# Kernel tuning notes

Measured on AMD Instinct MI355X. Metric: run time of the kernel, lower is better.

The kernel has to match this reference:

```python
import jax, jax.numpy as jnp
import numpy as np

V = 32000   # vocab
D = 512     # embed dim
H = 512     # hidden dim
K = 5       # beam size
SOS, EOS, PAD = 0, 1, 2
NEG = -1e30  # acts as -inf but keeps grads NaN-free


def gru_cell(x, h, Wih, Whh, bih, bhh):
    # torch nn.GRU cell convention: gates ordered (r, z, n)
    gi = x @ Wih.T + bih
    gh = h @ Whh.T + bhh
    i_r, i_z, i_n = jnp.split(gi, 3, axis=-1)
    h_r, h_z, h_n = jnp.split(gh, 3, axis=-1)
    r = jax.nn.sigmoid(i_r + h_r)
    z = jax.nn.sigmoid(i_z + h_z)
    n = jnp.tanh(i_n + r * h_n)
    return (1.0 - z) * n + z * h


def setup_inputs() -> dict:
    key = jax.random.key(0)
    ks = jax.random.split(key, 14)
    s = 0.02
    f = jnp.float32
    return {
        "source": jax.random.randint(ks[0], (32, 32), 0, V, dtype=jnp.int32),
        "emb_src": jax.random.normal(ks[1], (V, D), f) * s,
        "emb_tgt": jax.random.normal(ks[2], (V, D), f) * s,
        "enc_Wih": jax.random.normal(ks[3], (3 * H, D), f) * s,
        "enc_Whh": jax.random.normal(ks[4], (3 * H, H), f) * s,
        "enc_bih": jnp.zeros((3 * H,), f),
        "enc_bhh": jnp.zeros((3 * H,), f),
        "dec_Wih": jax.random.normal(ks[5], (3 * H, D), f) * s,
        "dec_Whh": jax.random.normal(ks[6], (3 * H, H), f) * s,
        "dec_bih": jnp.zeros((3 * H,), f),
        "dec_bhh": jnp.zeros((3 * H,), f),
        "W_out": jax.random.normal(ks[7], (H, V), f) * s,
        "b_out": jnp.zeros((V,), f),
    }


def beam_search(source, emb_src, emb_tgt, enc_Wih, enc_Whh, enc_bih, enc_bhh,
                dec_Wih, dec_Whh, dec_bih, dec_bhh, W_out, b_out):
    B, S = source.shape
    T = S + 1  # max decode steps (while counter < source.shape[1] + 1)

    # ---- encoder: 1-layer GRU over source tokens ----
    xs = jnp.swapaxes(emb_src[source], 0, 1)  # [S, B, D]
    def enc_step(h, x):
        return gru_cell(x, h, enc_Wih, enc_Whh, enc_bih, enc_bhh), None
    h_enc, _ = jax.lax.scan(enc_step, jnp.zeros((B, H), xs.dtype), xs)
    # initialize_h: repeat each sentence's hidden state beam_size times
    hidden = jnp.broadcast_to(h_enc[:, None, :], (B, K, H))  # [B, K, H]

    def dec_logprobs(tok, hid):
        x = emb_tgt[tok]  # [B, K, D]
        h1 = gru_cell(x, hid, dec_Wih, dec_Whh, dec_bih, dec_bhh)
        lp = jax.nn.log_softmax(h1 @ W_out + b_out, axis=-1)  # [B, K, V]
        return lp, h1

    # ---- step 0: initial_advance (top-K words from one SOS row) ----
    lp, h1 = dec_logprobs(jnp.zeros((B, K), jnp.int32), hidden)
    vals, words = jax.lax.top_k(lp[:, 0, :], K)  # [B, K]
    seqs = jnp.full((B, K, T + 1), PAD, jnp.int32)
    seqs = seqs.at[:, :, 0].set(SOS).at[:, :, 1].set(words)
    act_ll = vals
    hidden = h1  # all beams identical at step 0
    best_ll = jnp.full((B,), NEG, vals.dtype)
    best_seq = jnp.full((B, T + 1), PAD, jnp.int32)
    pos = jnp.arange(T + 1)
    bidx = jnp.arange(B)

    # ---- steps 1..T-1: advance. Dead beam slots carry NEG likelihood,
    # which reproduces the shrinking-active-set math of the original. ----
    def step(carry, t):
        seqs, act_ll, hidden, last_tok, best_ll, best_seq = carry
        lp, h1 = dec_logprobs(last_tok, hidden)
        L = (act_ll[:, :, None] + lp).reshape(B, K * V)
        vals, idx = jax.lax.top_k(L, K)
        parent = idx // V           # seq_ind
        word = idx % V              # word_ind
        gathered = jnp.take_along_axis(seqs, parent[:, :, None], axis=1)
        new_seqs = jnp.where(pos[None, None, :] == t + 1, word[:, :, None], gathered)
        finite = vals > NEG * 0.5
        is_eos = (word == EOS) & finite
        # completed likelihood normalized by candidate length (t+2 tokens)
        comp_ll = jnp.where(is_eos, vals / (t.astype(vals.dtype) + 2.0), NEG)
        cbest = comp_ll.max(axis=1)
        cseq = new_seqs[bidx, comp_ll.argmax(axis=1)]  # [B, T+1], PAD-padded
        improve = cbest > best_ll
        best_ll = jnp.where(improve, cbest, best_ll)
        best_seq = jnp.where(improve[:, None], cseq, best_seq)
        act_ll = jnp.where(finite & ~is_eos, vals, NEG)
        hidden = jnp.take_along_axis(h1, parent[:, :, None], axis=1)  # arrange_h gather
        return (new_seqs, act_ll, hidden, word, best_ll, best_seq), None

    carry = (seqs, act_ll, hidden, words, best_ll, best_seq)
    carry, _ = jax.lax.scan(step, carry, jnp.arange(1, T))
    seqs, act_ll, hidden, last_tok, best_ll, best_seq = carry

    # return_winner: best completed if any, else best active
    have = best_ll > NEG * 0.5
    act_best = act_ll.argmax(axis=1)
    act_seq = seqs[bidx, act_best]
    winner = jnp.where(have[:, None], best_seq, act_seq)  # [B, T+1]
    winner_ll = jnp.where(have, best_ll, act_ll.max(axis=1))
    return winner, winner_ll


def reference(source, emb_src, emb_tgt, enc_Wih, enc_Whh, enc_bih, enc_bhh,
              dec_Wih, dec_Whh, dec_bih, dec_bhh, W_out, b_out):
    winner, _ = beam_search(source, emb_src, emb_tgt, enc_Wih, enc_Whh, enc_bih,
                            enc_bhh, dec_Wih, dec_Whh, dec_bih, dec_bhh, W_out, b_out)
    return winner
```

## Files before the change

### kernel.cpp

```cpp
#include <hip/hip_runtime.h>
#include <math.h>

#define NEGF   (-1e30f)
#define FINTH  (-5e29f)
#define VSZ    32000
#define KBM    5
#define SEQL   34
#define NVBLK  1000

__device__ __forceinline__ bool cand_gt(float av, int ai, float bv, int bi) {
  return (av > bv) || (av == bv && ai < bi);
}

#define INS5(xx, ii)                                                           \
  if (cand_gt(xx, ii, tv4, ti4)) {                                             \
    tv4 = xx; ti4 = ii;                                                        \
    if (cand_gt(tv4, ti4, tv3, ti3)) { float tf = tv3; int tj = ti3; tv3 = tv4; ti3 = ti4; tv4 = tf; ti4 = tj; \
      if (cand_gt(tv3, ti3, tv2, ti2)) { tf = tv2; tj = ti2; tv2 = tv3; ti2 = ti3; tv3 = tf; ti3 = tj; \
        if (cand_gt(tv2, ti2, tv1, ti1)) { tf = tv1; tj = ti1; tv1 = tv2; ti1 = ti2; tv2 = tf; ti2 = tj; \
          if (cand_gt(tv1, ti1, tv0, ti0)) { tf = tv0; tj = ti0; tv0 = tv1; ti0 = ti1; tv1 = tf; ti1 = tj; } } } } }

__global__ void init_kernel(float* hb0, int* word_buf, int* hsrc) {
  int i = blockIdx.x * 256 + threadIdx.x;
  if (i < 32 * 512) hb0[i] = 0.f;
  if (i < 160) { word_buf[i] = 0; hsrc[i] = i / KBM; }
}

__global__ __launch_bounds__(256, 4) void genc_kernel(
    const float* __restrict__ emb, const int* __restrict__ source,
    const float* __restrict__ Wih, float* __restrict__ gi_enc)
{
  const int tid = threadIdx.x;
  const int ng = tid & 7;
  const int mg = tid >> 3;
  const int j0 = blockIdx.x * 16 + ng * 2;
  const int r0 = blockIdx.y * 128 + mg * 4;

  const float* arow[4];
  #pragma unroll
  for (int i = 0; i < 4; i++) {
    int r = r0 + i;
    int tok = source[(r & 31) * 32 + (r >> 5)];
    arow[i] = emb + (long)tok * 512;
  }
  const float* w0p = Wih + (long)j0 * 512;
  const float* w1p = w0p + 512;

  float acc0[4], acc1[4];
  #pragma unroll
  for (int i = 0; i < 4; i++) { acc0[i] = 0.f; acc1[i] = 0.f; }

  float4 wc0 = *(const float4*)w0p;
  float4 wc1 = *(const float4*)w1p;
  float4 ac[4];
  #pragma unroll
  for (int i = 0; i < 4; i++) ac[i] = *(const float4*)arow[i];

  for (int k = 0; k < 508; k += 4) {
    float4 wn0 = *(const float4*)(w0p + k + 4);
    float4 wn1 = *(const float4*)(w1p + k + 4);
    float4 an[4];
    #pragma unroll
    for (int i = 0; i < 4; i++) an[i] = *(const float4*)(arow[i] + k + 4);
    #pragma unroll
    for (int i = 0; i < 4; i++) {
      acc0[i] += ac[i].x * wc0.x + ac[i].y * wc0.y + ac[i].z * wc0.z + ac[i].w * wc0.w;
      acc1[i] += ac[i].x * wc1.x + ac[i].y * wc1.y + ac[i].z * wc1.z + ac[i].w * wc1.w;
    }
    wc0 = wn0; wc1 = wn1;
    #pragma unroll
    for (int i = 0; i < 4; i++) ac[i] = an[i];
  }
  #pragma unroll
  for (int i = 0; i < 4; i++) {
    acc0[i] += ac[i].x * wc0.x + ac[i].y * wc0.y + ac[i].z * wc0.z + ac[i].w * wc0.w;
    acc1[i] += ac[i].x * wc1.x + ac[i].y * wc1.y + ac[i].z * wc1.z + ac[i].w * wc1.w;
  }
  #pragma unroll
  for (int i = 0; i < 4; i++) {
    float2 r; r.x = acc0[i]; r.y = acc1[i];
    *(float2*)(gi_enc + (long)(r0 + i) * 1536 + j0) = r;
  }
}

template<int P, int HONLY>
__global__ __launch_bounds__(256, 4) void gates_kernel(
    const float* __restrict__ emb, const int* __restrict__ tok_ptr, int tok_stride,
    const float* __restrict__ hbuf, const int* __restrict__ hsrc,
    const float* __restrict__ Wih, const float* __restrict__ Whh,
    float* __restrict__ gip, float* __restrict__ ghp)
{
  const bool is_h = HONLY ? true : (blockIdx.y != 0);
  const float* W = is_h ? Whh : Wih;
  const int M = 32 * P;
  float* out = (is_h ? ghp : gip) + (long)blockIdx.z * M * 1536;

  const int tid = threadIdx.x;
  const int ng = tid & 7;
  const int mg = tid >> 3;
  const int j0 = blockIdx.x * 16 + ng * 2;
  const int k0 = blockIdx.z * 128;

  const float* arow[P];
  #pragma unroll
  for (int i = 0; i < P; i++) {
    int m = mg * P + i;
    if (is_h) { int r = hsrc ? hsrc[m] : m; arow[i] = hbuf + (long)r * 512 + k0; }
    else      { int tk = tok_ptr[m * tok_stride]; arow[i] = emb + (long)tk * 512 + k0; }
  }
  const float* w0p = W + (long)j0 * 512 + k0;
  const float* w1p = w0p + 512;

  float acc0[P], acc1[P];
  #pragma unroll
  for (int i = 0; i < P; i++) { acc0[i] = 0.f; acc1[i] = 0.f; }

  float4 wc0 = *(const float4*)w0p;
  float4 wc1 = *(const float4*)w1p;
  float4 ac[P];
  #pragma unroll
  for (int i = 0; i < P; i++) ac[i] = *(const float4*)arow[i];

  for (int k = 0; k < 124; k += 4) {
    float4 wn0 = *(const float4*)(w0p + k + 4);
    float4 wn1 = *(const float4*)(w1p + k + 4);
    float4 an[P];
    #pragma unroll
    for (int i = 0; i < P; i++) an[i] = *(const float4*)(arow[i] + k + 4);
    #pragma unroll
    for (int i = 0; i < P; i++) {
      acc0[i] += ac[i].x * wc0.x + ac[i].y * wc0.y + ac[i].z * wc0.z + ac[i].w * wc0.w;
      acc1[i] += ac[i].x * wc1.x + ac[i].y * wc1.y + ac[i].z * wc1.z + ac[i].w * wc1.w;
    }
    wc0 = wn0; wc1 = wn1;
    #pragma unroll
    for (int i = 0; i < P; i++) ac[i] = an[i];
  }
  #pragma unroll
  for (int i = 0; i < P; i++) {
    acc0[i] += ac[i].x * wc0.x + ac[i].y * wc0.y + ac[i].z * wc0.z + ac[i].w * wc0.w;
    acc1[i] += ac[i].x * wc1.x + ac[i].y * wc1.y + ac[i].z * wc1.z + ac[i].w * wc1.w;
  }
  #pragma unroll
  for (int i = 0; i < P; i++) {
    int m = mg * P + i;
    float2 r; r.x = acc0[i]; r.y = acc1[i];
    *(float2*)(out + (long)m * 1536 + j0) = r;
  }
}

template<int NPI, int NPH, int M>
__global__ __launch_bounds__(256) void hupd_kernel(
    const float* __restrict__ gip, const float* __restrict__ ghp,
    const float* __restrict__ bih, const float* __restrict__ bhh,
    const float* __restrict__ hin, const int* __restrict__ hsrc,
    float* __restrict__ hout)
{
  int idx = blockIdx.x * 256 + threadIdx.x;
  if (idx >= M * 512) return;
  int m = idx >> 9, i = idx & 511;
  float ir = 0.f, iz = 0.f, inn = 0.f, hr = 0.f, hz = 0.f, hn = 0.f;
  #pragma unroll
  for (int p = 0; p < NPI; p++) {
    const float* g = gip + (long)p * M * 1536 + (long)m * 1536;
    ir += g[i]; iz += g[512 + i]; inn += g[1024 + i];
  }
  #pragma unroll
  for (int p = 0; p < NPH; p++) {
    const float* g = ghp + (long)p * M * 1536 + (long)m * 1536;
    hr += g[i]; hz += g[512 + i]; hn += g[1024 + i];
  }
  ir += bih[i]; iz += bih[512 + i]; inn += bih[1024 + i];
  hr += bhh[i]; hz += bhh[512 + i]; hn += bhh[1024 + i];
  float r = 1.f / (1.f + expf(-(ir + hr)));
  float z = 1.f / (1.f + expf(-(iz + hz)));
  float n = tanhf(inn + r * hn);
  int src = hsrc ? hsrc[m] : m;
  float h = hin[(long)src * 512 + i];
  hout[(long)m * 512 + i] = (1.f - z) * n + z * h;
}

__global__ __launch_bounds__(256, 4) void logtop_kernel(
    const float* __restrict__ h1, const float* __restrict__ Wout,
    const float* __restrict__ bout,
    float* __restrict__ pms, float* __restrict__ pv, int* __restrict__ pi)
{
  const int tid = threadIdx.x;
  const int ng = tid & 7;
  const int mg = tid >> 3;
  const int blk = blockIdx.x;
  const int v0 = blk * 32;
  const int v = v0 + ng * 4;
  const int m0 = mg * 5;

  __shared__ float Wlds[2][2048];
  __shared__ float L[160][33];

  const float* a0 = h1 + (long)m0 * 512;

  const int skk = tid >> 3;
  const int sv4 = tid & 7;
  const float* sg0 = Wout + (size_t)skk * VSZ + v0 + sv4 * 4;
  const float* sg1 = Wout + (size_t)(32 + skk) * VSZ + v0 + sv4 * 4;
  const int lwave = (tid >> 6) * 256;

  auto stage = [&](int tt, int bb) {
    const float* g0 = sg0 + (size_t)tt * 64 * VSZ;
    const float* g1 = sg1 + (size_t)tt * 64 * VSZ;
    __builtin_amdgcn_global_load_lds(
        (const __attribute__((address_space(1))) void*)g0,
        (__attribute__((address_space(3))) void*)&Wlds[bb][lwave], 16, 0, 0);
    __builtin_amdgcn_global_load_lds(
        (const __attribute__((address_space(1))) void*)g1,
        (__attribute__((address_space(3))) void*)&Wlds[bb][1024 + lwave], 16, 0, 0);
  };

  float4 acc[5];
  #pragma unroll
  for (int i = 0; i < 5; i++) acc[i] = make_float4(0.f, 0.f, 0.f, 0.f);

  stage(0, 0);
  __syncthreads();

  float4 aA[5], aB[5];
  #pragma unroll
  for (int i = 0; i < 5; i++) aA[i] = *(const float4*)(a0 + i * 512);

  for (int t8 = 0; t8 < 8; t8++) {
    const float* lb = &Wlds[t8 & 1][0];
    if (t8 < 7) stage(t8 + 1, (t8 + 1) & 1);
    const int kt = t8 * 64;
    #pragma unroll 1
    for (int c = 0; c < 16; c += 2) {
      const int k = kt + c * 4;
      float4 w0[4], w1[4];
      #pragma unroll
      for (int j = 0; j < 4; j++) w0[j] = *(const float4*)&lb[(c * 4 + j) * 32 + ng * 4];
      #pragma unroll
      for (int j = 0; j < 4; j++) w1[j] = *(const float4*)&lb[(c * 4 + 4 + j) * 32 + ng * 4];
      #pragma unroll
      for (int i = 0; i < 5; i++) aB[i] = *(const float4*)(a0 + i * 512 + k + 4);
      #pragma unroll
      for (int i = 0; i < 5; i++) {
        acc[i].x += aA[i].x * w0[0].x + aA[i].y * w0[1].x + aA[i].z * w0[2].x + aA[i].w * w0[3].x;
        acc[i].y += aA[i].x * w0[0].y + aA[i].y * w0[1].y + aA[i].z * w0[2].y + aA[i].w * w0[3].y;
        acc[i].z += aA[i].x * w0[0].z + aA[i].y * w0[1].z + aA[i].z * w0[2].z + aA[i].w * w0[3].z;
        acc[i].w += aA[i].x * w0[0].w + aA[i].y * w0[1].w + aA[i].z * w0[2].w + aA[i].w * w0[3].w;
      }
      int kn = k + 8; if (kn >= 512) kn = 0;
      #pragma unroll
      for (int i = 0; i < 5; i++) aA[i] = *(const float4*)(a0 + i * 512 + kn);
      #pragma unroll
      for (int i = 0; i < 5; i++) {
        acc[i].x += aB[i].x * w1[0].x + aB[i].y * w1[1].x + aB[i].z * w1[2].x + aB[i].w * w1[3].x;
        acc[i].y += aB[i].x * w1[0].y + aB[i].y * w1[1].y + aB[i].z * w1[2].y + aB[i].w * w1[3].y;
        acc[i].z += aB[i].x * w1[0].z + aB[i].y * w1[1].z + aB[i].z * w1[2].z + aB[i].w * w1[3].z;
        acc[i].w += aB[i].x * w1[0].w + aB[i].y * w1[1].w + aB[i].z * w1[2].w + aB[i].w * w1[3].w;
      }
    }
    __syncthreads();
  }

  float4 bb4 = *(const float4*)(bout + v);
  #pragma unroll
  for (int i = 0; i < 5; i++) {
    L[m0 + i][ng * 4 + 0] = acc[i].x + bb4.x;
    L[m0 + i][ng * 4 + 1] = acc[i].y + bb4.y;
    L[m0 + i][ng * 4 + 2] = acc[i].z + bb4.z;
    L[m0 + i][ng * 4 + 3] = acc[i].w + bb4.w;
  }
  __syncthreads();

  if (tid < 160) {
    float m = -3.4e38f, s = 0.f;
    float tv0 = -3.4e38f, tv1 = -3.4e38f, tv2 = -3.4e38f, tv3 = -3.4e38f, tv4 = -3.4e38f;
    int ti0 = 0x7fffffff, ti1 = 0x7fffffff, ti2 = 0x7fffffff, ti3 = 0x7fffffff, ti4 = 0x7fffffff;
    int base = blk * 32;
    for (int c = 0; c < 32; c++) {
      float x = L[tid][c];
      if (x > m) { s *= expf(m - x); m = x; }
      s += expf(x - m);
      INS5(x, base + c);
    }
    long o = (long)blk * 160 + tid;
    pms[o * 2 + 0] = m; pms[o * 2 + 1] = s;
    pv[o * 5 + 0] = tv0; pi[o * 5 + 0] = ti0;
    pv[o * 5 + 1] = tv1; pi[o * 5 + 1] = ti1;
    pv[o * 5 + 2] = tv2; pi[o * 5 + 2] = ti2;
    pv[o * 5 + 3] = tv3; pi[o * 5 + 3] = ti3;
    pv[o * 5 + 4] = tv4; pi[o * 5 + 4] = ti4;
  }
}

__global__ __launch_bounds__(256) void merge_kernel(
    const float* __restrict__ pms, const float* __restrict__ pv,
    const int* __restrict__ pi, float* __restrict__ lse,
    float* __restrict__ rv5, int* __restrict__ ri5)
{
  int row = blockIdx.x, tid = threadIdx.x;
  float m = -3.4e38f, s = 0.f;
  float tv0 = -3.4e38f, tv1 = -3.4e38f, tv2 = -3.4e38f, tv3 = -3.4e38f, tv4 = -3.4e38f;
  int ti0 = 0x7fffffff, ti1 = 0x7fffffff, ti2 = 0x7fffffff, ti3 = 0x7fffffff, ti4 = 0x7fffffff;

  for (int blk = tid; blk < NVBLK; blk += 256) {
    long o = (long)blk * 160 + row;
    float bm = pms[o * 2 + 0], bs = pms[o * 2 + 1];
    float nm = fmaxf(m, bm);
    s = s * expf(m - nm) + bs * expf(bm - nm);
    m = nm;
    float xv; int xi;
    xv = pv[o * 5 + 0]; xi = pi[o * 5 + 0]; INS5(xv, xi);
    xv = pv[o * 5 + 1]; xi = pi[o * 5 + 1]; INS5(xv, xi);
    xv = pv[o * 5 + 2]; xi = pi[o * 5 + 2]; INS5(xv, xi);
    xv = pv[o * 5 + 3]; xi = pi[o * 5 + 3]; INS5(xv, xi);
    xv = pv[o * 5 + 4]; xi = pi[o * 5 + 4]; INS5(xv, xi);
  }
  for (int mask = 1; mask < 64; mask <<= 1) {
    float om = __shfl_xor(m, mask, 64);
    float os = __shfl_xor(s, mask, 64);
    float nm = fmaxf(m, om);
    s = s * expf(m - nm) + os * expf(om - nm);
    m = nm;
  }
  __shared__ float sm[4], ss[4];
  __shared__ float sv[256 * 5];
  __shared__ int   si[256 * 5];
  if ((tid & 63) == 0) { sm[tid >> 6] = m; ss[tid >> 6] = s; }
  sv[tid * 5 + 0] = tv0; si[tid * 5 + 0] = ti0;
  sv[tid * 5 + 1] = tv1; si[tid * 5 + 1] = ti1;
  sv[tid * 5 + 2] = tv2; si[tid * 5 + 2] = ti2;
  sv[tid * 5 + 3] = tv3; si[tid * 5 + 3] = ti3;
  sv[tid * 5 + 4] = tv4; si[tid * 5 + 4] = ti4;
  __syncthreads();
  if (tid == 0) {
    float M2 = sm[0], S2 = ss[0];
    for (int w = 1; w < 4; w++) {
      float nm = fmaxf(M2, sm[w]);
      S2 = S2 * expf(M2 - nm) + ss[w] * expf(sm[w] - nm);
      M2 = nm;
    }
    lse[row] = M2 + logf(S2);
  }
  for (int str = 128; str >= 1; str >>= 1) {
    if (tid < str) {
      float* av = &sv[tid * 5];         int* ai = &si[tid * 5];
      float* bv = &sv[(tid + str) * 5]; int* bi = &si[(tid + str) * 5];
      float o0[5]; int o1[5];
      int i = 0, j = 0;
      #pragma unroll
      for (int o = 0; o < 5; o++) {
        float avv = av[i]; int aii = ai[i];
        float bvv = bv[j]; int bii = bi[j];
        bool ta = cand_gt(avv, aii, bvv, bii);
        o0[o] = ta ? avv : bvv; o1[o] = ta ? aii : bii;
        i += ta ? 1 : 0; j += ta ? 0 : 1;
      }
      #pragma unroll
      for (int o = 0; o < 5; o++) { av[o] = o0[o]; ai[o] = o1[o]; }
    }
    __syncthreads();
  }
  if (tid == 0) {
    #pragma unroll
    for (int o = 0; o < 5; o++) { rv5[row * 5 + o] = sv[o]; ri5[row * 5 + o] = si[o]; }
  }
}

__global__ void book0_kernel(const float* __restrict__ rv5, const int* __restrict__ ri5,
                             const float* __restrict__ lse,
                             int* __restrict__ seqs, float* __restrict__ act_ll,
                             int* __restrict__ word_buf, int* __restrict__ hsrc,
                             float* __restrict__ best_ll, int* __restrict__ best_seq)
{
  int b = blockIdx.x, tid = threadIdx.x;
  int row = b * KBM;
  float l = lse[row];
  if (tid < SEQL) {
    for (int j = 0; j < KBM; j++) {
      int w = ri5[row * 5 + j];
      seqs[(b * KBM + j) * SEQL + tid] = (tid == 0) ? 0 : (tid == 1 ? w : 2);
    }
    best_seq[b * SEQL + tid] = 2;
  }
  if (tid < KBM) {
    act_ll[b * KBM + tid] = rv5[row * 5 + tid] - l;
    word_buf[b * KBM + tid] = ri5[row * 5 + tid];
    hsrc[b * KBM + tid] = b * KBM + tid;
  }
  if (tid == 0) best_ll[b] = NEGF;
}

__global__ void book_kernel(const float* __restrict__ rv5, const int* __restrict__ ri5,
                            const float* __restrict__ lse,
                            const int* __restrict__ seqs_old, int* __restrict__ seqs_new,
                            float* __restrict__ act_ll, int* __restrict__ word_buf,
                            int* __restrict__ hsrc, float* __restrict__ best_ll,
                            int* __restrict__ best_seq, int t)
{
  int b = blockIdx.x, tid = threadIdx.x;
  __shared__ float sv5[5];
  __shared__ int   si5[5];
  if (tid == 0) {
    float tv0 = -3.4e38f, tv1 = -3.4e38f, tv2 = -3.4e38f, tv3 = -3.4e38f, tv4 = -3.4e38f;
    int ti0 = 0x7fffffff, ti1 = 0x7fffffff, ti2 = 0x7fffffff, ti3 = 0x7fffffff, ti4 = 0x7fffffff;
    for (int k = 0; k < KBM; k++) {
      int row = b * KBM + k;
      float a = act_ll[row], l = lse[row];
      #pragma unroll
      for (int j = 0; j < 5; j++) {
        float x = a + (rv5[row * 5 + j] - l);
        int id = k * VSZ + ri5[row * 5 + j];
        INS5(x, id);
      }
    }
    sv5[0] = tv0; si5[0] = ti0; sv5[1] = tv1; si5[1] = ti1;
    sv5[2] = tv2; si5[2] = ti2; sv5[3] = tv3; si5[3] = ti3;
    sv5[4] = tv4; si5[4] = ti4;
  }
  __syncthreads();

  __shared__ int ls[KBM][SEQL];
  float v[KBM]; int pr[KBM], wd[KBM];
  #pragma unroll
  for (int j = 0; j < KBM; j++) {
    v[j] = sv5[j];
    int id = si5[j];
    pr[j] = id / VSZ; wd[j] = id % VSZ;
  }
  #pragma unroll
  for (int j = 0; j < KBM; j++) {
    if (tid < SEQL) {
      int x = (tid == t + 1) ? wd[j] : seqs_old[(b * KBM + pr[j]) * SEQL + tid];
      ls[j][tid] = x;
      seqs_new[(b * KBM + j) * SEQL + tid] = x;
    }
  }
  __syncthreads();
  float cll[KBM];
  #pragma unroll
  for (int j = 0; j < KBM; j++) {
    bool fin = v[j] > FINTH;
    bool eos = (wd[j] == 1) && fin;
    cll[j] = eos ? v[j] / (float)(t + 2) : NEGF;
  }
  int jb = 0; float cb = cll[0];
  #pragma unroll
  for (int j = 1; j < KBM; j++) if (cll[j] > cb) { cb = cll[j]; jb = j; }
  bool improve = cb > best_ll[b];
  if (improve) {
    if (tid == 0) best_ll[b] = cb;
    if (tid < SEQL) best_seq[b * SEQL + tid] = ls[jb][tid];
  }
  if (tid < KBM) {
    int j = tid;
    bool fin = v[j] > FINTH;
    bool eos = (wd[j] == 1) && fin;
    act_ll[b * KBM + j] = (fin && !eos) ? v[j] : NEGF;
    word_buf[b * KBM + j] = wd[j];
    hsrc[b * KBM + j] = b * KBM + pr[j];
  }
}

__global__ void final_kernel(const float* __restrict__ best_ll, const int* __restrict__ best_seq,
                             const float* __restrict__ act_ll, const int* __restrict__ seqs,
                             int* __restrict__ out)
{
  int b = blockIdx.x, tid = threadIdx.x;
  bool have = best_ll[b] > FINTH;
  int jb = 0; float ab = act_ll[b * KBM];
  for (int j = 1; j < KBM; j++)
    if (act_ll[b * KBM + j] > ab) { ab = act_ll[b * KBM + j]; jb = j; }
  if (tid < SEQL)
    out[b * SEQL + tid] = have ? best_seq[b * SEQL + tid]
                               : seqs[(b * KBM + jb) * SEQL + tid];
}

extern "C" void kernel_launch(void* const* d_in, const int* in_sizes, int n_in,
                              void* d_out, int out_size, void* d_ws, size_t ws_size,
                              hipStream_t stream)
{
  const int*   source  = (const int*)d_in[0];
  const float* emb_src = (const float*)d_in[1];
  const float* emb_tgt = (const float*)d_in[2];
  const float* eWih = (const float*)d_in[3];
  const float* eWhh = (const float*)d_in[4];
  const float* ebih = (const float*)d_in[5];
  const float* ebhh = (const float*)d_in[6];
  const float* dWih = (const float*)d_in[7];
  const float* dWhh = (const float*)d_in[8];
  const float* dbih = (const float*)d_in[9];
  const float* dbhh = (const float*)d_in[10];
  const float* Wout = (const float*)d_in[11];
  const float* bout = (const float*)d_in[12];
  int* out = (int*)d_out;

  char* ws = (char*)d_ws;
  size_t off = 0;
  auto alloc = [&](size_t bytes) {
    void* p = ws + off;
    off = (off + bytes + 255) & ~(size_t)255;
    return p;
  };
  float* hb0     = (float*)alloc(160 * 512 * 4);
  float* hb1     = (float*)alloc(160 * 512 * 4);
  float* gip     = (float*)alloc((size_t)4 * 160 * 1536 * 4);
  float* ghp     = (float*)alloc((size_t)4 * 160 * 1536 * 4);
  char*  uni     = (char*) alloc((size_t)8 * 1024 * 1024);
  float* gi_enc  = (float*)uni;
  float* pms     = (float*)uni;
  float* pv      = (float*)(uni + 1536 * 1024);
  int*   pi      = (int*)  (uni + 1536 * 1024 + 3328 * 1024);
  float* lse     = (float*)alloc(160 * 4);
  float* act_ll  = (float*)alloc(160 * 4);
  float* rv5     = (float*)alloc(160 * 5 * 4);
  float* best_ll = (float*)alloc(32 * 4);
  int*   ri5     = (int*)alloc(160 * 5 * 4);
  int*   seqs0   = (int*)alloc(160 * SEQL * 4);
  int*   seqs1   = (int*)alloc(160 * SEQL * 4);
  int*   wordb   = (int*)alloc(160 * 4);
  int*   hsrc    = (int*)alloc(160 * 4);
  int*   bseq    = (int*)alloc(32 * SEQL * 4);

  init_kernel<<<64, 256, 0, stream>>>(hb0, wordb, hsrc);

  genc_kernel<<<dim3(96, 8), 256, 0, stream>>>(emb_src, source, eWih, gi_enc);
  for (int s = 0; s < 32; s++) {
    gates_kernel<1, 1><<<dim3(96, 1, 4), 256, 0, stream>>>(
        nullptr, nullptr, 0, hb0, nullptr, nullptr, eWhh, nullptr, ghp);
    hupd_kernel<1, 4, 32><<<64, 256, 0, stream>>>(
        gi_enc + (size_t)s * 32 * 1536, ghp, ebih, ebhh, hb0, nullptr, hb0);
  }

  gates_kernel<5, 0><<<dim3(96, 2, 4), 256, 0, stream>>>(
      emb_tgt, wordb, 1, hb0, hsrc, dWih, dWhh, gip, ghp);
  hupd_kernel<4, 4, 160><<<320, 256, 0, stream>>>(
      gip, ghp, dbih, dbhh, hb0, hsrc, hb1);
  logtop_kernel<<<NVBLK, 256, 0, stream>>>(hb1, Wout, bout, pms, pv, pi);
  merge_kernel<<<160, 256, 0, stream>>>(pms, pv, pi, lse, rv5, ri5);
  book0_kernel<<<32, 64, 0, stream>>>(rv5, ri5, lse, seqs0, act_ll, wordb, hsrc,
                                      best_ll, bseq);

  float* hcur = hb1; float* hoth = hb0;
  int* scur = seqs0; int* soth = seqs1;
  for (int t = 1; t <= 32; t++) {
    gates_kernel<5, 0><<<dim3(96, 2, 4), 256, 0, stream>>>(
        emb_tgt, wordb, 1, hcur, hsrc, dWih, dWhh, gip, ghp);
    hupd_kernel<4, 4, 160><<<320, 256, 0, stream>>>(
        gip, ghp, dbih, dbhh, hcur, hsrc, hoth);
    logtop_kernel<<<NVBLK, 256, 0, stream>>>(hoth, Wout, bout, pms, pv, pi);
    merge_kernel<<<160, 256, 0, stream>>>(pms, pv, pi, lse, rv5, ri5);
    book_kernel<<<32, 64, 0, stream>>>(rv5, ri5, lse, scur, soth, act_ll, wordb,
                                       hsrc, best_ll, bseq, t);
    { float* tmp = hcur; hcur = hoth; hoth = tmp; }
    { int* tmp = scur; scur = soth; soth = tmp; }
  }

  final_kernel<<<32, 64, 0, stream>>>(best_ll, bseq, act_ll, scur, out);
}
```

Measured before the change: 6.886 ms.

## Fuse merge and beam bookkeeping into one kernel with packed partials

Merges the per-row top-5/logsumexp reduction kernel and the beam bookkeeping kernel into a single per-sentence kernel, using wave shuffles for the reduction instead of a shared-memory tree. The logits kernel now writes its partials as a packed 16-float record per row, read back with float4 loads. This removes one launch per decode step and the intermediate lse/top-5 buffers. The trade-off is only 32 blocks doing the merge work, each handling 5 rows per thread. The encoder input-projection kernel also gets half the rows per thread and twice the grid.

New measurement: 10.30 ms. 49.5% more time.

```diff
diff --git a/kernel.cpp b/kernel.cpp
--- a/kernel.cpp
+++ b/kernel.cpp
@@ -20,6 +20,41 @@
         if (cand_gt(tv2, ti2, tv1, ti1)) { tf = tv1; tj = ti1; tv1 = tv2; ti1 = ti2; tv2 = tf; ti2 = tj; \
           if (cand_gt(tv1, ti1, tv0, ti0)) { tf = tv0; tj = ti0; tv0 = tv1; ti0 = ti1; tv1 = tf; ti1 = tj; } } } } }
 
+struct T5 { float v[5]; int i[5]; };
+
+__device__ __forceinline__ void t5_init(T5& t) {
+  #pragma unroll
+  for (int j = 0; j < 5; j++) { t.v[j] = -3.4e38f; t.i[j] = 0x7fffffff; }
+}
+
+__device__ __forceinline__ void t5_ins(T5& t, float x, int id) {
+  if (cand_gt(x, id, t.v[4], t.i[4])) {
+    t.v[4] = x; t.i[4] = id;
+    #pragma unroll
+    for (int j = 4; j > 0; j--) {
+      if (cand_gt(t.v[j], t.i[j], t.v[j-1], t.i[j-1])) {
+        float tf = t.v[j-1]; int tj = t.i[j-1];
+        t.v[j-1] = t.v[j]; t.i[j-1] = t.i[j];
+        t.v[j] = tf; t.i[j] = tj;
+      }
+    }
+  }
+}
+
+__device__ __forceinline__ T5 t5_merge(const T5& a, const T5& b) {
+  T5 r;
+  int i = 0, j = 0;
+  #pragma unroll
+  for (int o = 0; o < 5; o++) {
+    float avv = a.v[i]; int aii = a.i[i];
+    float bvv = b.v[j]; int bii = b.i[j];
+    bool ta = cand_gt(avv, aii, bvv, bii);
+    r.v[o] = ta ? avv : bvv; r.i[o] = ta ? aii : bii;
+    i += ta ? 1 : 0; j += ta ? 0 : 1;
+  }
+  return r;
+}
+
 __global__ void init_kernel(float* hb0, int* word_buf, int* hsrc) {
   int i = blockIdx.x * 256 + threadIdx.x;
   if (i < 32 * 512) hb0[i] = 0.f;
@@ -34,11 +69,11 @@
   const int ng = tid & 7;
   const int mg = tid >> 3;
   const int j0 = blockIdx.x * 16 + ng * 2;
-  const int r0 = blockIdx.y * 128 + mg * 4;
-
-  const float* arow[4];
-  #pragma unroll
-  for (int i = 0; i < 4; i++) {
+  const int r0 = blockIdx.y * 64 + mg * 2;
+
+  const float* arow[2];
+  #pragma unroll
+  for (int i = 0; i < 2; i++) {
     int r = r0 + i;
     int tok = source[(r & 31) * 32 + (r >> 5)];
     arow[i] = emb + (long)tok * 512;
@@ -46,38 +81,38 @@
   const float* w0p = Wih + (long)j0 * 512;
   const float* w1p = w0p + 512;
 
-  float acc0[4], acc1[4];
-  #pragma unroll
-  for (int i = 0; i < 4; i++) { acc0[i] = 0.f; acc1[i] = 0.f; }
+  float acc0[2], acc1[2];
+  #pragma unroll
+  for (int i = 0; i < 2; i++) { acc0[i] = 0.f; acc1[i] = 0.f; }
 
   float4 wc0 = *(const float4*)w0p;
   float4 wc1 = *(const float4*)w1p;
-  float4 ac[4];
-  #pragma unroll
-  for (int i = 0; i < 4; i++) ac[i] = *(const float4*)arow[i];
+  float4 ac[2];
+  #pragma unroll
+  for (int i = 0; i < 2; i++) ac[i] = *(const float4*)arow[i];
 
   for (int k = 0; k < 508; k += 4) {
     float4 wn0 = *(const float4*)(w0p + k + 4);
     float4 wn1 = *(const float4*)(w1p + k + 4);
-    float4 an[4];
-    #pragma unroll
-    for (int i = 0; i < 4; i++) an[i] = *(const float4*)(arow[i] + k + 4);
-    #pragma unroll
-    for (int i = 0; i < 4; i++) {
+    float4 an[2];
+    #pragma unroll
+    for (int i = 0; i < 2; i++) an[i] = *(const float4*)(arow[i] + k + 4);
+    #pragma unroll
+    for (int i = 0; i < 2; i++) {
       acc0[i] += ac[i].x * wc0.x + ac[i].y * wc0.y + ac[i].z * wc0.z + ac[i].w * wc0.w;
       acc1[i] += ac[i].x * wc1.x + ac[i].y * wc1.y + ac[i].z * wc1.z + ac[i].w * wc1.w;
     }
     wc0 = wn0; wc1 = wn1;
     #pragma unroll
-    for (int i = 0; i < 4; i++) ac[i] = an[i];
-  }
-  #pragma unroll
-  for (int i = 0; i < 4; i++) {
+    for (int i = 0; i < 2; i++) ac[i] = an[i];
+  }
+  #pragma unroll
+  for (int i = 0; i < 2; i++) {
     acc0[i] += ac[i].x * wc0.x + ac[i].y * wc0.y + ac[i].z * wc0.z + ac[i].w * wc0.w;
     acc1[i] += ac[i].x * wc1.x + ac[i].y * wc1.y + ac[i].z * wc1.z + ac[i].w * wc1.w;
   }
   #pragma unroll
-  for (int i = 0; i < 4; i++) {
+  for (int i = 0; i < 2; i++) {
     float2 r; r.x = acc0[i]; r.y = acc1[i];
     *(float2*)(gi_enc + (long)(r0 + i) * 1536 + j0) = r;
   }
@@ -182,8 +217,7 @@
 
 __global__ __launch_bounds__(256, 4) void logtop_kernel(
     const float* __restrict__ h1, const float* __restrict__ Wout,
-    const float* __restrict__ bout,
-    float* __restrict__ pms, float* __restrict__ pv, int* __restrict__ pi)
+    const float* __restrict__ bout, float* __restrict__ PK)
 {
   const int tid = threadIdx.x;
   const int ng = tid & 7;
@@ -282,182 +316,178 @@
       s += expf(x - m);
       INS5(x, base + c);
     }
-    long o = (long)blk * 160 + tid;
-    pms[o * 2 + 0] = m; pms[o * 2 + 1] = s;
-    pv[o * 5 + 0] = tv0; pi[o * 5 + 0] = ti0;
-    pv[o * 5 + 1] = tv1; pi[o * 5 + 1] = ti1;
-    pv[o * 5 + 2] = tv2; pi[o * 5 + 2] = ti2;
-    pv[o * 5 + 3] = tv3; pi[o * 5 + 3] = ti3;
-    pv[o * 5 + 4] = tv4; pi[o * 5 + 4] = ti4;
-  }
-}
-
-__global__ __launch_bounds__(256) void merge_kernel(
-    const float* __restrict__ pms, const float* __restrict__ pv,
-    const int* __restrict__ pi, float* __restrict__ lse,
-    float* __restrict__ rv5, int* __restrict__ ri5)
-{
-  int row = blockIdx.x, tid = threadIdx.x;
-  float m = -3.4e38f, s = 0.f;
-  float tv0 = -3.4e38f, tv1 = -3.4e38f, tv2 = -3.4e38f, tv3 = -3.4e38f, tv4 = -3.4e38f;
-  int ti0 = 0x7fffffff, ti1 = 0x7fffffff, ti2 = 0x7fffffff, ti3 = 0x7fffffff, ti4 = 0x7fffffff;
-
-  for (int blk = tid; blk < NVBLK; blk += 256) {
-    long o = (long)blk * 160 + row;
-    float bm = pms[o * 2 + 0], bs = pms[o * 2 + 1];
-    float nm = fmaxf(m, bm);
-    s = s * expf(m - nm) + bs * expf(bm - nm);
-    m = nm;
-    float xv; int xi;
-    xv = pv[o * 5 + 0]; xi = pi[o * 5 + 0]; INS5(xv, xi);
-    xv = pv[o * 5 + 1]; xi = pi[o * 5 + 1]; INS5(xv, xi);
-    xv = pv[o * 5 + 2]; xi = pi[o * 5 + 2]; INS5(xv, xi);
-    xv = pv[o * 5 + 3]; xi = pi[o * 5 + 3]; INS5(xv, xi);
-    xv = pv[o * 5 + 4]; xi = pi[o * 5 + 4]; INS5(xv, xi);
-  }
-  for (int mask = 1; mask < 64; mask <<= 1) {
-    float om = __shfl_xor(m, mask, 64);
-    float os = __shfl_xor(s, mask, 64);
-    float nm = fmaxf(m, om);
-    s = s * expf(m - nm) + os * expf(om - nm);
-    m = nm;
-  }
-  __shared__ float sm[4], ss[4];
-  __shared__ float sv[256 * 5];
-  __shared__ int   si[256 * 5];
-  if ((tid & 63) == 0) { sm[tid >> 6] = m; ss[tid >> 6] = s; }
-  sv[tid * 5 + 0] = tv0; si[tid * 5 + 0] = ti0;
-  sv[tid * 5 + 1] = tv1; si[tid * 5 + 1] = ti1;
-  sv[tid * 5 + 2] = tv2; si[tid * 5 + 2] = ti2;
-  sv[tid * 5 + 3] = tv3; si[tid * 5 + 3] = ti3;
-  sv[tid * 5 + 4] = tv4; si[tid * 5 + 4] = ti4;
-  __syncthreads();
-  if (tid == 0) {
-    float M2 = sm[0], S2 = ss[0];
-    for (int w = 1; w < 4; w++) {
-      float nm = fmaxf(M2, sm[w]);
-      S2 = S2 * expf(M2 - nm) + ss[w] * expf(sm[w] - nm);
-      M2 = nm;
-    }
-    lse[row] = M2 + logf(S2);
-  }
-  for (int str = 128; str >= 1; str >>= 1) {
-    if (tid < str) {
-      float* av = &sv[tid * 5];         int* ai = &si[tid * 5];
-      float* bv = &sv[(tid + str) * 5]; int* bi = &si[(tid + str) * 5];
-      float o0[5]; int o1[5];
-      int i = 0, j = 0;
-      #pragma unroll
-      for (int o = 0; o < 5; o++) {
-        float avv = av[i]; int aii = ai[i];
-        float bvv = bv[j]; int bii = bi[j];
-        bool ta = cand_gt(avv, aii, bvv, bii);
-        o0[o] = ta ? avv : bvv; o1[o] = ta ? aii : bii;
-        i += ta ? 1 : 0; j += ta ? 0 : 1;
-      }
-      #pragma unroll
-      for (int o = 0; o < 5; o++) { av[o] = o0[o]; ai[o] = o1[o]; }
-    }
-    __syncthreads();
-  }
-  if (tid == 0) {
-    #pragma unroll
-    for (int o = 0; o < 5; o++) { rv5[row * 5 + o] = sv[o]; ri5[row * 5 + o] = si[o]; }
-  }
-}
-
-__global__ void book0_kernel(const float* __restrict__ rv5, const int* __restrict__ ri5,
-                             const float* __restrict__ lse,
-                             int* __restrict__ seqs, float* __restrict__ act_ll,
-                             int* __restrict__ word_buf, int* __restrict__ hsrc,
-                             float* __restrict__ best_ll, int* __restrict__ best_seq)
-{
-  int b = blockIdx.x, tid = threadIdx.x;
-  int row = b * KBM;
-  float l = lse[row];
-  if (tid < SEQL) {
-    for (int j = 0; j < KBM; j++) {
-      int w = ri5[row * 5 + j];
-      seqs[(b * KBM + j) * SEQL + tid] = (tid == 0) ? 0 : (tid == 1 ? w : 2);
-    }
-    best_seq[b * SEQL + tid] = 2;
-  }
-  if (tid < KBM) {
-    act_ll[b * KBM + tid] = rv5[row * 5 + tid] - l;
-    word_buf[b * KBM + tid] = ri5[row * 5 + tid];
-    hsrc[b * KBM + tid] = b * KBM + tid;
-  }
-  if (tid == 0) best_ll[b] = NEGF;
-}
-
-__global__ void book_kernel(const float* __restrict__ rv5, const int* __restrict__ ri5,
-                            const float* __restrict__ lse,
-                            const int* __restrict__ seqs_old, int* __restrict__ seqs_new,
-                            float* __restrict__ act_ll, int* __restrict__ word_buf,
-                            int* __restrict__ hsrc, float* __restrict__ best_ll,
-                            int* __restrict__ best_seq, int t)
-{
-  int b = blockIdx.x, tid = threadIdx.x;
+    float* pk = PK + ((long)blk * 160 + tid) * 16;
+    float4 q0 = make_float4(m, s, tv0, tv1);
+    float4 q1 = make_float4(tv2, tv3, tv4, __int_as_float(ti0));
+    float4 q2 = make_float4(__int_as_float(ti1), __int_as_float(ti2),
+                            __int_as_float(ti3), __int_as_float(ti4));
+    *(float4*)(pk + 0) = q0;
+    *(float4*)(pk + 4) = q1;
+    *(float4*)(pk + 8) = q2;
+  }
+}
+
+template<int NR>
+__global__ __launch_bounds__(256) void mergebook_kernel(
+    const float* __restrict__ PK,
+    const int* __restrict__ seqs_old, int* __restrict__ seqs_new,
+    float* __restrict__ act_ll, int* __restrict__ word_buf,
+    int* __restrict__ hsrc, float* __restrict__ best_ll,
+    int* __restrict__ best_seq, int t)
+{
+  const int b = blockIdx.x, tid = threadIdx.x;
+
+  float m_[NR], s_[NR];
+  T5 t5[NR];
+  #pragma unroll
+  for (int k = 0; k < NR; k++) { m_[k] = -3.4e38f; s_[k] = 0.f; t5_init(t5[k]); }
+
+  for (int it = 0; it < 4; it++) {
+    int blk = tid + it * 256;
+    if (blk >= NVBLK) break;
+    #pragma unroll
+    for (int k = 0; k < NR; k++) {
+      const float* pk = PK + ((long)blk * 160 + b * KBM + k) * 16;
+      float4 q0 = *(const float4*)(pk + 0);
+      float4 q1 = *(const float4*)(pk + 4);
+      float4 q2 = *(const float4*)(pk + 8);
+      float nm = fmaxf(m_[k], q0.x);
+      s_[k] = s_[k] * expf(m_[k] - nm) + q0.y * expf(q0.x - nm);
+      m_[k] = nm;
+      t5_ins(t5[k], q0.z, __float_as_int(q1.w));
+      t5_ins(t5[k], q0.w, __float_as_int(q2.x));
+      t5_ins(t5[k], q1.x, __float_as_int(q2.y));
+      t5_ins(t5[k], q1.y, __float_as_int(q2.z));
+      t5_ins(t5[k], q1.z, __float_as_int(q2.w));
+    }
+  }
+
+  #pragma unroll
+  for (int k = 0; k < NR; k++) {
+    float m = m_[k], s = s_[k];
+    for (int mask = 1; mask < 64; mask <<= 1) {
+      float om = __shfl_xor(m, mask, 64);
+      float os = __shfl_xor(s, mask, 64);
+      float nm = fmaxf(m, om);
+      s = s * expf(m - nm) + os * expf(om - nm);
+      m = nm;
+    }
+    m_[k] = m; s_[k] = s;
+    for (int mask = 1; mask < 64; mask <<= 1) {
+      T5 o;
+      #pragma unroll
+      for (int j = 0; j < 5; j++) {
+        o.v[j] = __shfl_xor(t5[k].v[j], mask, 64);
+        o.i[j] = __shfl_xor(t5[k].i[j], mask, 64);
+      }
+      t5[k] = t5_merge(t5[k], o);
+    }
+  }
+
+  __shared__ float wm[KBM][4], wss[KBM][4], wv[KBM][4][5];
+  __shared__ int   wi[KBM][4][5];
   __shared__ float sv5[5];
   __shared__ int   si5[5];
+  const int wave = tid >> 6;
+  if ((tid & 63) == 0) {
+    #pragma unroll
+    for (int k = 0; k < NR; k++) {
+      wm[k][wave] = m_[k]; wss[k][wave] = s_[k];
+      #pragma unroll
+      for (int j = 0; j < 5; j++) { wv[k][wave][j] = t5[k].v[j]; wi[k][wave][j] = t5[k].i[j]; }
+    }
+  }
+  __syncthreads();
+
   if (tid == 0) {
-    float tv0 = -3.4e38f, tv1 = -3.4e38f, tv2 = -3.4e38f, tv3 = -3.4e38f, tv4 = -3.4e38f;
-    int ti0 = 0x7fffffff, ti1 = 0x7fffffff, ti2 = 0x7fffffff, ti3 = 0x7fffffff, ti4 = 0x7fffffff;
-    for (int k = 0; k < KBM; k++) {
-      int row = b * KBM + k;
-      float a = act_ll[row], l = lse[row];
+    T5 g; t5_init(g);
+    #pragma unroll
+    for (int k = 0; k < NR; k++) {
+      float M2 = wm[k][0], S2 = wss[k][0];
+      #pragma unroll
+      for (int w = 1; w < 4; w++) {
+        float nm = fmaxf(M2, wm[k][w]);
+        S2 = S2 * expf(M2 - nm) + wss[k][w] * expf(wm[k][w] - nm);
+        M2 = nm;
+      }
+      float l = M2 + logf(S2);
+      T5 rk;
+      #pragma unroll
+      for (int j = 0; j < 5; j++) { rk.v[j] = wv[k][0][j]; rk.i[j] = wi[k][0][j]; }
+      #pragma unroll
+      for (int w = 1; w < 4; w++) {
+        T5 o;
+        #pragma unroll
+        for (int j = 0; j < 5; j++) { o.v[j] = wv[k][w][j]; o.i[j] = wi[k][w][j]; }
+        rk = t5_merge(rk, o);
+      }
+      float a = (NR == 1) ? 0.f : act_ll[b * KBM + k];
       #pragma unroll
       for (int j = 0; j < 5; j++) {
-        float x = a + (rv5[row * 5 + j] - l);
-        int id = k * VSZ + ri5[row * 5 + j];
-        INS5(x, id);
-      }
-    }
-    sv5[0] = tv0; si5[0] = ti0; sv5[1] = tv1; si5[1] = ti1;
-    sv5[2] = tv2; si5[2] = ti2; sv5[3] = tv3; si5[3] = ti3;
-    sv5[4] = tv4; si5[4] = ti4;
+        t5_ins(g, a + (rk.v[j] - l), k * VSZ + rk.i[j]);
+      }
+    }
+    #pragma unroll
+    for (int j = 0; j < 5; j++) { sv5[j] = g.v[j]; si5[j] = g.i[j]; }
   }
   __syncthreads();
 
-  __shared__ int ls[KBM][SEQL];
-  float v[KBM]; int pr[KBM], wd[KBM];
-  #pragma unroll
-  for (int j = 0; j < KBM; j++) {
-    v[j] = sv5[j];
-    int id = si5[j];
-    pr[j] = id / VSZ; wd[j] = id % VSZ;
-  }
-  #pragma unroll
-  for (int j = 0; j < KBM; j++) {
+  if (NR == 1) {
     if (tid < SEQL) {
-      int x = (tid == t + 1) ? wd[j] : seqs_old[(b * KBM + pr[j]) * SEQL + tid];
-      ls[j][tid] = x;
-      seqs_new[(b * KBM + j) * SEQL + tid] = x;
-    }
-  }
-  __syncthreads();
-  float cll[KBM];
-  #pragma unroll
-  for (int j = 0; j < KBM; j++) {
-    bool fin = v[j] > FINTH;
-    bool eos = (wd[j] == 1) && fin;
-    cll[j] = eos ? v[j] / (float)(t + 2) : NEGF;
-  }
-  int jb = 0; float cb = cll[0];
-  #pragma unroll
-  for (int j = 1; j < KBM; j++) if (cll[j] > cb) { cb = cll[j]; jb = j; }
-  bool improve = cb > best_ll[b];
-  if (improve) {
-    if (tid == 0) best_ll[b] = cb;
-    if (tid < SEQL) best_seq[b * SEQL + tid] = ls[jb][tid];
-  }
-  if (tid < KBM) {
-    int j = tid;
-    bool fin = v[j] > FINTH;
-    bool eos = (wd[j] == 1) && fin;
-    act_ll[b * KBM + j] = (fin && !eos) ? v[j] : NEGF;
-    word_buf[b * KBM + j] = wd[j];
-    hsrc[b * KBM + j] = b * KBM + pr[j];
+      #pragma unroll
+      for (int j = 0; j < KBM; j++) {
+        int w = si5[j];
+        seqs_new[(b * KBM + j) * SEQL + tid] = (tid == 0) ? 0 : (tid == 1 ? w : 2);
+      }
+      best_seq[b * SEQL + tid] = 2;
+    }
+    if (tid < KBM) {
+      act_ll[b * KBM + tid] = sv5[tid];
+      word_buf[b * KBM + tid] = si5[tid];
+      hsrc[b * KBM + tid] = b * KBM + tid;
+    }
+    if (tid == 0) best_ll[b] = NEGF;
+  } else {
+    __shared__ int ls[KBM][SEQL];
+    float v[KBM]; int pr[KBM], wd[KBM];
+    #pragma unroll
+    for (int j = 0; j < KBM; j++) {
+      v[j] = sv5[j];
+      int id = si5[j];
+      pr[j] = id / VSZ; wd[j] = id % VSZ;
+    }
+    #pragma unroll
+    for (int j = 0; j < KBM; j++) {
+      if (tid < SEQL) {
+        int x = (tid == t + 1) ? wd[j] : seqs_old[(b * KBM + pr[j]) * SEQL + tid];
+        ls[j][tid] = x;
+        seqs_new[(b * KBM + j) * SEQL + tid] = x;
+      }
+    }
+    __syncthreads();
+    float cll[KBM];
+    #pragma unroll
+    for (int j = 0; j < KBM; j++) {
+      bool fin = v[j] > FINTH;
+      bool eos = (wd[j] == 1) && fin;
+      cll[j] = eos ? v[j] / (float)(t + 2) : NEGF;
+    }
+    int jb = 0; float cb = cll[0];
+    #pragma unroll
+    for (int j = 1; j < KBM; j++) if (cll[j] > cb) { cb = cll[j]; jb = j; }
+    bool improve = cb > best_ll[b];
+    if (improve) {
+      if (tid == 0) best_ll[b] = cb;
+      if (tid < SEQL) best_seq[b * SEQL + tid] = ls[jb][tid];
+    }
+    if (tid < KBM) {
+      int j = tid;
+      bool fin = v[j] > FINTH;
+      bool eos = (wd[j] == 1) && fin;
+      act_ll[b * KBM + j] = (fin && !eos) ? v[j] : NEGF;
+      word_buf[b * KBM + j] = wd[j];
+      hsrc[b * KBM + j] = b * KBM + pr[j];
+    }
   }
 }
 
@@ -505,16 +535,11 @@
   float* hb1     = (float*)alloc(160 * 512 * 4);
   float* gip     = (float*)alloc((size_t)4 * 160 * 1536 * 4);
   float* ghp     = (float*)alloc((size_t)4 * 160 * 1536 * 4);
-  char*  uni     = (char*) alloc((size_t)8 * 1024 * 1024);
+  char*  uni     = (char*) alloc((size_t)11 * 1024 * 1024);
   float* gi_enc  = (float*)uni;
-  float* pms     = (float*)uni;
-  float* pv      = (float*)(uni + 1536 * 1024);
-  int*   pi      = (int*)  (uni + 1536 * 1024 + 3328 * 1024);
-  float* lse     = (float*)alloc(160 * 4);
+  float* PK      = (float*)uni;
   float* act_ll  = (float*)alloc(160 * 4);
-  float* rv5     = (float*)alloc(160 * 5 * 4);
   float* best_ll = (float*)alloc(32 * 4);
-  int*   ri5     = (int*)alloc(160 * 5 * 4);
   int*   seqs0   = (int*)alloc(160 * SEQL * 4);
   int*   seqs1   = (int*)alloc(160 * SEQL * 4);
   int*   wordb   = (int*)alloc(160 * 4);
@@ -523,7 +548,7 @@
 
   init_kernel<<<64, 256, 0, stream>>>(hb0, wordb, hsrc);
 
-  genc_kernel<<<dim3(96, 8), 256, 0, stream>>>(emb_src, source, eWih, gi_enc);
+  genc_kernel<<<dim3(96, 16), 256, 0, stream>>>(emb_src, source, eWih, gi_enc);
   for (int s = 0; s < 32; s++) {
     gates_kernel<1, 1><<<dim3(96, 1, 4), 256, 0, stream>>>(
         nullptr, nullptr, 0, hb0, nullptr, nullptr, eWhh, nullptr, ghp);
@@ -535,10 +560,9 @@
       emb_tgt, wordb, 1, hb0, hsrc, dWih, dWhh, gip, ghp);
   hupd_kernel<4, 4, 160><<<320, 256, 0, stream>>>(
       gip, ghp, dbih, dbhh, hb0, hsrc, hb1);
-  logtop_kernel<<<NVBLK, 256, 0, stream>>>(hb1, Wout, bout, pms, pv, pi);
-  merge_kernel<<<160, 256, 0, stream>>>(pms, pv, pi, lse, rv5, ri5);
-  book0_kernel<<<32, 64, 0, stream>>>(rv5, ri5, lse, seqs0, act_ll, wordb, hsrc,
-                                      best_ll, bseq);
+  logtop_kernel<<<NVBLK, 256, 0, stream>>>(hb1, Wout, bout, PK);
+  mergebook_kernel<1><<<32, 256, 0, stream>>>(PK, seqs0, seqs0, act_ll, wordb,
+                                              hsrc, best_ll, bseq, 0);
 
   float* hcur = hb1; float* hoth = hb0;
   int* scur = seqs0; int* soth = seqs1;
@@ -547,10 +571,9 @@
         emb_tgt, wordb, 1, hcur, hsrc, dWih, dWhh, gip, ghp);
     hupd_kernel<4, 4, 160><<<320, 256, 0, stream>>>(
         gip, ghp, dbih, dbhh, hcur, hsrc, hoth);
-    logtop_kernel<<<NVBLK, 256, 0, stream>>>(hoth, Wout, bout, pms, pv, pi);
-    merge_kernel<<<160, 256, 0, stream>>>(pms, pv, pi, lse, rv5, ri5);
-    book_kernel<<<32, 64, 0, stream>>>(rv5, ri5, lse, scur, soth, act_ll, wordb,
-                                       hsrc, best_ll, bseq, t);
+    logtop_kernel<<<NVBLK, 256, 0, stream>>>(hoth, Wout, bout, PK);
+    mergebook_kernel<5><<<32, 256, 0, stream>>>(PK, scur, soth, act_ll, wordb,
+                                                hsrc, best_ll, bseq, t);
     { float* tmp = hcur; hcur = hoth; hoth = tmp; }
     { int* tmp = scur; scur = soth; soth = tmp; }
   }
```
